# Optimization experiments

Hardware: AMD Instinct MI355X
Metric: run time of the kernel (lower is better)

Reference implementation:

```python
import jax, jax.numpy as jnp
import numpy as np


def setup_inputs() -> dict:
    key = jax.random.key(0)
    k1, k2 = jax.random.split(key)
    # [batch, seq, in_features] activations
    x = jax.random.normal(k1, (4, 4096, 2048), dtype=jnp.float32)
    # fp32 master weight [out_features, in_features]; quantized inside reference
    weight = jax.random.normal(k2, (2048, 2048), dtype=jnp.float32) * 0.02
    return {"x": x, "weight": weight}


def reference(x, weight):
    num_bits = 8
    Qn = -(2 ** (num_bits - 1))       # -128
    Qp = 2 ** (num_bits - 1) - 1      # 127

    # Per-row absmax int8 activation quantization (activation_quant)
    si = Qp / jnp.clip(jnp.max(jnp.abs(x), axis=-1, keepdims=True), 1e-5)  # [B,S,1]
    qx = jnp.clip(jnp.round(x * si), Qn, Qp)  # int8 values held in fp32 (exact)

    # Ternary weight quantization (weight_quant): sw scalar = 1/mean|W|
    sw = 1.0 / jnp.clip(jnp.mean(jnp.abs(weight)), 1e-5)
    qw = jnp.clip(jnp.round(weight * sw), -1.0, 1.0)  # {-1,0,1}

    acc = jnp.einsum("bsk,nk->bsn", qx, qw)  # [B,S,out]

    # post_quant_process: dequantize by si and sw, cast to half
    out = ((acc / si) / sw).astype(jnp.float16)
    return out
```

## Files before the change

kernel.cpp:

```cpp
#include <hip/hip_runtime.h>

#define K_DIM 2048
#define N_DIM 2048
#define M_DIM 16384

typedef int v4i __attribute__((ext_vector_type(4)));
typedef int v16i __attribute__((ext_vector_type(16)));


__device__ __forceinline__ void lds16(const void* g, void* l) {
    __builtin_amdgcn_global_load_lds(
        (const __attribute__((address_space(1))) unsigned int*)g,
        (__attribute__((address_space(3))) unsigned int*)l,
        16, 0, 0);
}

__global__ __launch_bounds__(256) void k_wsum(const float* __restrict__ w,
                                              double* __restrict__ part) {
    int tid = blockIdx.x * 256 + threadIdx.x;
    const float4* w4 = (const float4*)w;
    double s = 0.0;
    for (int i = tid; i < (N_DIM * K_DIM / 4); i += 65536) {
        float4 v = w4[i];
        s += (double)fabsf(v.x);
        s += (double)fabsf(v.y);
        s += (double)fabsf(v.z);
        s += (double)fabsf(v.w);
    }
#pragma unroll
    for (int off = 32; off; off >>= 1) s += __shfl_xor(s, off, 64);
    __shared__ double sp[4];
    int lane = threadIdx.x & 63, wv = threadIdx.x >> 6;
    if (lane == 0) sp[wv] = s;
    __syncthreads();
    if (threadIdx.x == 0) part[blockIdx.x] = sp[0] + sp[1] + sp[2] + sp[3];
}

__global__ __launch_bounds__(256) void k_quant_w(const float* __restrict__ w,
                                                 signed char* __restrict__ qw_t,
                                                 const double* __restrict__ part,
                                                 float* __restrict__ invsw_out) {
    double s = part[threadIdx.x];
#pragma unroll
    for (int off = 32; off; off >>= 1) s += __shfl_xor(s, off, 64);
    __shared__ double sp[4];
    __shared__ float s_invsw;
    int lane = threadIdx.x & 63, wv = threadIdx.x >> 6;
    if (lane == 0) sp[wv] = s;
    __syncthreads();
    if (threadIdx.x == 0) {
        double total = sp[0] + sp[1] + sp[2] + sp[3];
        float mean = (float)(total * (1.0 / (double)(N_DIM * K_DIM)));
        s_invsw = fmaxf(mean, 1e-5f);
        if (blockIdx.x == 0) *invsw_out = s_invsw;
    }
    __syncthreads();
    float sw = 1.0f / s_invsw;

    int row = blockIdx.x * 4 + wv;
    const float4* wr_ = (const float4*)(w + (size_t)row * K_DIM);
    int bn = row >> 7, ri = row & 127;
    signed char* base = qw_t + (size_t)bn * 262144 + (((lane >> 2) & 3) << 11) + (ri << 4) + ((lane & 3) << 2);
    int ksBase = lane >> 4;
#pragma unroll
    for (int c = 0; c < 8; c++) {
        float4 v = wr_[c * 64 + lane];
        int q0 = (int)fminf(fmaxf(rintf(v.x * sw), -1.f), 1.f);
        int q1 = (int)fminf(fmaxf(rintf(v.y * sw), -1.f), 1.f);
        int q2 = (int)fminf(fmaxf(rintf(v.z * sw), -1.f), 1.f);
        int q3 = (int)fminf(fmaxf(rintf(v.w * sw), -1.f), 1.f);
        int q = (q0 & 255) | ((q1 & 255) << 8) | ((q2 & 255) << 16) | ((q3 & 255) << 24);
        *(int*)(base + (size_t)(4 * c + ksBase) * 8192) = q;
    }
}

__global__ __launch_bounds__(256) void k_quant_x(const float* __restrict__ x,
                                                 signed char* __restrict__ qx_t,
                                                 float* __restrict__ si_out) {
    int row = blockIdx.x * 4 + (threadIdx.x >> 6);
    int lane = threadIdx.x & 63;
    const float4* xr = (const float4*)(x + (size_t)row * K_DIM);
    float4 v[8];
    float mx = 0.f;
#pragma unroll
    for (int c = 0; c < 8; c++) {
        v[c] = xr[c * 64 + lane];
        mx = fmaxf(mx, fmaxf(fmaxf(fabsf(v[c].x), fabsf(v[c].y)),
                             fmaxf(fabsf(v[c].z), fabsf(v[c].w))));
    }
#pragma unroll
    for (int off = 32; off; off >>= 1) mx = fmaxf(mx, __shfl_xor(mx, off, 64));
    float si = 127.0f / fmaxf(mx, 1e-5f);
    if (lane == 0) si_out[row] = si;

    int bm = row >> 8, ri = row & 255;
    signed char* base = qx_t + (size_t)bm * 524288 + (((lane >> 2) & 3) << 12) + (ri << 4) + ((lane & 3) << 2);
    int ksBase = lane >> 4;
#pragma unroll
    for (int c = 0; c < 8; c++) {
        int q0 = (int)fminf(fmaxf(rintf(v[c].x * si), -128.f), 127.f);
        int q1 = (int)fminf(fmaxf(rintf(v[c].y * si), -128.f), 127.f);
        int q2 = (int)fminf(fmaxf(rintf(v[c].z * si), -128.f), 127.f);
        int q3 = (int)fminf(fmaxf(rintf(v[c].w * si), -128.f), 127.f);
        int q = (q0 & 255) | ((q1 & 255) << 8) | ((q2 & 255) << 16) | ((q3 & 255) << 24);
        *(int*)(base + (size_t)(4 * c + ksBase) * 16384) = q;
    }
}

__global__ __launch_bounds__(256, 2) void k_gemm(const signed char* __restrict__ qx_t,
                                                 const signed char* __restrict__ qw_t,
                                                 const float* __restrict__ si,
                                                 const float* __restrict__ invsw_p,
                                                 float* __restrict__ out) {
    __shared__ __align__(16) signed char As[3][16384];
    __shared__ __align__(16) signed char Bs[2][8192];
    const int t = threadIdx.x;
    const int lane = t & 63, wv = t >> 6;
    const int wr = wv >> 1, wc = wv & 1;
    const int l31 = lane & 31, lh = lane >> 5;

    const int wg = blockIdx.x;
    const int swz = (wg & 7) * 128 + (wg >> 3);
    const int bn = swz & 15, bm = swz >> 4;

    const signed char* aT = qx_t + (size_t)bm * 524288;
    const signed char* bT = qw_t + (size_t)bn * 262144;
    const int t16 = t << 4;

#define STAGE_A(buf, ksv)                                    \
    {                                                        \
        const signed char* aS = aT + ((size_t)(ksv) << 14);  \
        signed char* Ad = As[buf];                           \
        lds16(aS + t16,         Ad + t16);                   \
        lds16(aS + 4096 + t16,  Ad + 4096 + t16);            \
        lds16(aS + 8192 + t16,  Ad + 8192 + t16);            \
        lds16(aS + 12288 + t16, Ad + 12288 + t16);           \
    }
#define STAGE_B(buf, ksv)                                    \
    {                                                        \
        const signed char* bS = bT + ((size_t)(ksv) << 13);  \
        signed char* Bd = Bs[buf];                           \
        lds16(bS + t16,         Bd + t16);                   \
        lds16(bS + 4096 + t16,  Bd + 4096 + t16);            \
    }

    v16i acc[4][2] = {};

#define COMPUTE(AC, BC)                                                                              \
    {                                                                                                \
        const signed char* Ac = As[AC];                                                              \
        const signed char* Bc = Bs[BC];                                                              \
        _Pragma("unroll")                                                                            \
        for (int ks2 = 0; ks2 < 2; ks2++) {                                                          \
            v4i af[4], bf[2];                                                                        \
            _Pragma("unroll")                                                                        \
            for (int mt = 0; mt < 4; mt++)                                                           \
                af[mt] = *(const v4i*)(Ac + (((ks2 * 2 + lh) * 256 + wr * 128 + mt * 32 + l31) << 4)); \
            _Pragma("unroll")                                                                        \
            for (int nt = 0; nt < 2; nt++)                                                           \
                bf[nt] = *(const v4i*)(Bc + (((ks2 * 2 + lh) * 128 + wc * 64 + nt * 32 + l31) << 4)); \
            _Pragma("unroll")                                                                        \
            for (int mt = 0; mt < 4; mt++)                                                           \
                _Pragma("unroll")                                                                    \
                for (int nt = 0; nt < 2; nt++)                                                       \
                    acc[mt][nt] = __builtin_amdgcn_mfma_i32_32x32x32_i8(af[mt], bf[nt], acc[mt][nt], 0, 0, 0); \
        }                                                                                            \
    }

#define ITER10(ksv, AC, BC, AS, BS)                          \
    {                                                        \
        STAGE_B(BS, (ksv) + 1);                              \
        STAGE_A(AS, (ksv) + 2);                              \
        asm volatile("s_waitcnt vmcnt(10)" ::: "memory");    \
        __builtin_amdgcn_s_barrier();                        \
        COMPUTE(AC, BC);                                     \
        __builtin_amdgcn_s_barrier();                        \
    }

    STAGE_B(0, 0);
    STAGE_A(0, 0);
    STAGE_A(1, 1);

    for (int ks = 0; ks < 30; ks += 6) {
        ITER10(ks + 0, 0, 0, 2, 1);
        ITER10(ks + 1, 1, 1, 0, 0);
        ITER10(ks + 2, 2, 0, 1, 1);
        ITER10(ks + 3, 0, 1, 2, 0);
        ITER10(ks + 4, 1, 0, 0, 1);
        ITER10(ks + 5, 2, 1, 1, 0);
    }

    STAGE_B(1, 31);
    asm volatile("s_waitcnt vmcnt(6)" ::: "memory");
    __builtin_amdgcn_s_barrier();
    COMPUTE(0, 0);
    __builtin_amdgcn_s_barrier();
    asm volatile("s_waitcnt vmcnt(0)" ::: "memory");
    __builtin_amdgcn_s_barrier();
    COMPUTE(1, 1);

#undef ITER10
#undef COMPUTE
#undef STAGE_A
#undef STAGE_B

    float invsw = *invsw_p;
#pragma unroll
    for (int mt = 0; mt < 4; mt++) {
        int rowb = bm * 256 + wr * 128 + mt * 32 + (lh << 2);
        float sc[16];
#pragma unroll
        for (int r = 0; r < 16; r++)
            sc[r] = invsw / si[rowb + (r & 3) + ((r >> 2) << 3)];
#pragma unroll
        for (int nt = 0; nt < 2; nt++) {
            int col = bn * 128 + wc * 64 + nt * 32 + l31;
#pragma unroll
            for (int r = 0; r < 16; r++) {
                int row = rowb + (r & 3) + ((r >> 2) << 3);
                float vv = (float)acc[mt][nt][r] * sc[r];
                out[(size_t)row * N_DIM + col] = (float)(_Float16)vv;
            }
        }
    }
}

extern "C" void kernel_launch(void* const* d_in, const int* in_sizes, int n_in,
                              void* d_out, int out_size, void* d_ws, size_t ws_size,
                              hipStream_t stream) {
    const float* x = (const float*)d_in[0];
    const float* w = (const float*)d_in[1];
    float* out = (float*)d_out;
    char* ws = (char*)d_ws;

    double* part = (double*)ws;
    float* invsw = (float*)(ws + 2048);
    float* si = (float*)(ws + 4096);
    signed char* qw_t = (signed char*)(ws + 4096 + 65536);
    signed char* qx_t = qw_t + (size_t)N_DIM * K_DIM;

    k_wsum<<<256, 256, 0, stream>>>(w, part);
    k_quant_x<<<4096, 256, 0, stream>>>(x, qx_t, si);
    k_quant_w<<<512, 256, 0, stream>>>(w, qw_t, part, invsw);
    k_gemm<<<1024, 256, 0, stream>>>(qx_t, qw_t, si, invsw, out);
}
```

Before: 323.2 us.

## Interleave LDS reads with MFMA in GEMM, coalesce quant stores, widen wsum grid

The GEMM main loop now uses a single barrier per k-step. It splits each step into two halves so the next tile's global-to-LDS loads are issued between the LDS fragment reads and the MFMAs, and it raises wave priority around the MFMA groups. Both quantization kernels first stage packed int8 words in shared memory, then write them out as contiguous runs in the tiled layout instead of scattered 4-byte stores. The weight-sum kernel runs with 4x more blocks, and the reducer sums four partials per thread. Removing the trailing barrier relies on the vmcnt wait plus the buffer rotation to avoid read/write races on LDS buffers.

```diff
diff --git a/kernel.cpp b/kernel.cpp
--- a/kernel.cpp
+++ b/kernel.cpp
@@ -20,7 +20,7 @@
     int tid = blockIdx.x * 256 + threadIdx.x;
     const float4* w4 = (const float4*)w;
     double s = 0.0;
-    for (int i = tid; i < (N_DIM * K_DIM / 4); i += 65536) {
+    for (int i = tid; i < (N_DIM * K_DIM / 4); i += 262144) {
         float4 v = w4[i];
         s += (double)fabsf(v.x);
         s += (double)fabsf(v.y);
@@ -40,11 +40,13 @@
                                                  signed char* __restrict__ qw_t,
                                                  const double* __restrict__ part,
                                                  float* __restrict__ invsw_out) {
-    double s = part[threadIdx.x];
+    double s = part[threadIdx.x] + part[threadIdx.x + 256] +
+               part[threadIdx.x + 512] + part[threadIdx.x + 768];
 #pragma unroll
     for (int off = 32; off; off >>= 1) s += __shfl_xor(s, off, 64);
     __shared__ double sp[4];
     __shared__ float s_invsw;
+    __shared__ int lbuf[2048];
     int lane = threadIdx.x & 63, wv = threadIdx.x >> 6;
     if (lane == 0) sp[wv] = s;
     __syncthreads();
@@ -59,9 +61,7 @@
 
     int row = blockIdx.x * 4 + wv;
     const float4* wr_ = (const float4*)(w + (size_t)row * K_DIM);
-    int bn = row >> 7, ri = row & 127;
-    signed char* base = qw_t + (size_t)bn * 262144 + (((lane >> 2) & 3) << 11) + (ri << 4) + ((lane & 3) << 2);
-    int ksBase = lane >> 4;
+    int k16 = (lane >> 2) & 3, b = lane & 3, ksBase = lane >> 4;
 #pragma unroll
     for (int c = 0; c < 8; c++) {
         float4 v = wr_[c * 64 + lane];
@@ -70,15 +70,28 @@
         int q2 = (int)fminf(fmaxf(rintf(v.z * sw), -1.f), 1.f);
         int q3 = (int)fminf(fmaxf(rintf(v.w * sw), -1.f), 1.f);
         int q = (q0 & 255) | ((q1 & 255) << 8) | ((q2 & 255) << 16) | ((q3 & 255) << 24);
-        *(int*)(base + (size_t)(4 * c + ksBase) * 8192) = q;
+        int ks = 4 * c + ksBase;
+        lbuf[(ks * 4 + k16) * 16 + wv * 4 + b] = q;
+    }
+    __syncthreads();
+    int bn = (blockIdx.x * 4) >> 7, ri0 = (blockIdx.x * 4) & 127;
+    int* qdst = (int*)(qw_t + (size_t)bn * 262144 + (size_t)ri0 * 16);
+#pragma unroll
+    for (int r = 0; r < 8; r++) {
+        int chunk = r * 16 + (threadIdx.x >> 4);
+        int i16 = threadIdx.x & 15;
+        int ks = chunk >> 2, kk = chunk & 3;
+        int row4 = i16 >> 2, bb = i16 & 3;
+        qdst[ks * 2048 + kk * 512 + row4 * 4 + bb] = lbuf[chunk * 16 + i16];
     }
 }
 
 __global__ __launch_bounds__(256) void k_quant_x(const float* __restrict__ x,
                                                  signed char* __restrict__ qx_t,
                                                  float* __restrict__ si_out) {
-    int row = blockIdx.x * 4 + (threadIdx.x >> 6);
-    int lane = threadIdx.x & 63;
+    __shared__ int lbuf[2048];
+    int wv = threadIdx.x >> 6, lane = threadIdx.x & 63;
+    int row = blockIdx.x * 4 + wv;
     const float4* xr = (const float4*)(x + (size_t)row * K_DIM);
     float4 v[8];
     float mx = 0.f;
@@ -93,9 +106,7 @@
     float si = 127.0f / fmaxf(mx, 1e-5f);
     if (lane == 0) si_out[row] = si;
 
-    int bm = row >> 8, ri = row & 255;
-    signed char* base = qx_t + (size_t)bm * 524288 + (((lane >> 2) & 3) << 12) + (ri << 4) + ((lane & 3) << 2);
-    int ksBase = lane >> 4;
+    int k16 = (lane >> 2) & 3, b = lane & 3, ksBase = lane >> 4;
 #pragma unroll
     for (int c = 0; c < 8; c++) {
         int q0 = (int)fminf(fmaxf(rintf(v[c].x * si), -128.f), 127.f);
@@ -103,7 +114,19 @@
         int q2 = (int)fminf(fmaxf(rintf(v[c].z * si), -128.f), 127.f);
         int q3 = (int)fminf(fmaxf(rintf(v[c].w * si), -128.f), 127.f);
         int q = (q0 & 255) | ((q1 & 255) << 8) | ((q2 & 255) << 16) | ((q3 & 255) << 24);
-        *(int*)(base + (size_t)(4 * c + ksBase) * 16384) = q;
+        int ks = 4 * c + ksBase;
+        lbuf[(ks * 4 + k16) * 16 + wv * 4 + b] = q;
+    }
+    __syncthreads();
+    int bm = (blockIdx.x * 4) >> 8, ri0 = (blockIdx.x * 4) & 255;
+    int* qdst = (int*)(qx_t + (size_t)bm * 524288 + (size_t)ri0 * 16);
+#pragma unroll
+    for (int r = 0; r < 8; r++) {
+        int chunk = r * 16 + (threadIdx.x >> 4);
+        int i16 = threadIdx.x & 15;
+        int ks = chunk >> 2, kk = chunk & 3;
+        int row4 = i16 >> 2, bb = i16 & 3;
+        qdst[ks * 4096 + kk * 1024 + row4 * 4 + bb] = lbuf[chunk * 16 + i16];
     }
 }
 
@@ -146,35 +169,31 @@
 
     v16i acc[4][2] = {};
 
-#define COMPUTE(AC, BC)                                                                              \
-    {                                                                                                \
-        const signed char* Ac = As[AC];                                                              \
-        const signed char* Bc = Bs[BC];                                                              \
-        _Pragma("unroll")                                                                            \
-        for (int ks2 = 0; ks2 < 2; ks2++) {                                                          \
-            v4i af[4], bf[2];                                                                        \
-            _Pragma("unroll")                                                                        \
-            for (int mt = 0; mt < 4; mt++)                                                           \
-                af[mt] = *(const v4i*)(Ac + (((ks2 * 2 + lh) * 256 + wr * 128 + mt * 32 + l31) << 4)); \
-            _Pragma("unroll")                                                                        \
-            for (int nt = 0; nt < 2; nt++)                                                           \
-                bf[nt] = *(const v4i*)(Bc + (((ks2 * 2 + lh) * 128 + wc * 64 + nt * 32 + l31) << 4)); \
-            _Pragma("unroll")                                                                        \
-            for (int mt = 0; mt < 4; mt++)                                                           \
-                _Pragma("unroll")                                                                    \
-                for (int nt = 0; nt < 2; nt++)                                                       \
-                    acc[mt][nt] = __builtin_amdgcn_mfma_i32_32x32x32_i8(af[mt], bf[nt], acc[mt][nt], 0, 0, 0); \
-        }                                                                                            \
-    }
-
-#define ITER10(ksv, AC, BC, AS, BS)                          \
+#define READ_HALF(AC, BC, h, af, bf)                                                                 \
+    _Pragma("unroll") for (int mt = 0; mt < 4; mt++)                                                 \
+        af[mt] = *(const v4i*)(As[AC] + ((((h) * 2 + lh) * 256 + wr * 128 + mt * 32 + l31) << 4));   \
+    _Pragma("unroll") for (int nt = 0; nt < 2; nt++)                                                 \
+        bf[nt] = *(const v4i*)(Bs[BC] + ((((h) * 2 + lh) * 128 + wc * 64 + nt * 32 + l31) << 4));
+
+#define MFMA8(af, bf)                                                                                \
+    __builtin_amdgcn_s_setprio(1);                                                                   \
+    _Pragma("unroll") for (int mt = 0; mt < 4; mt++)                                                 \
+        _Pragma("unroll") for (int nt = 0; nt < 2; nt++)                                             \
+            acc[mt][nt] = __builtin_amdgcn_mfma_i32_32x32x32_i8(af[mt], bf[nt], acc[mt][nt], 0, 0, 0); \
+    __builtin_amdgcn_s_setprio(0);
+
+#define ITER(ksv, AC, BC, AS, BS)                            \
     {                                                        \
+        asm volatile("s_waitcnt vmcnt(4)" ::: "memory");     \
+        __builtin_amdgcn_s_barrier();                        \
+        __builtin_amdgcn_sched_barrier(0);                   \
+        v4i af[4], bf[2];                                    \
+        READ_HALF(AC, BC, 0, af, bf);                        \
         STAGE_B(BS, (ksv) + 1);                              \
+        MFMA8(af, bf);                                       \
+        READ_HALF(AC, BC, 1, af, bf);                        \
         STAGE_A(AS, (ksv) + 2);                              \
-        asm volatile("s_waitcnt vmcnt(10)" ::: "memory");    \
-        __builtin_amdgcn_s_barrier();                        \
-        COMPUTE(AC, BC);                                     \
-        __builtin_amdgcn_s_barrier();                        \
+        MFMA8(af, bf);                                       \
     }
 
     STAGE_B(0, 0);
@@ -182,25 +201,39 @@
     STAGE_A(1, 1);
 
     for (int ks = 0; ks < 30; ks += 6) {
-        ITER10(ks + 0, 0, 0, 2, 1);
-        ITER10(ks + 1, 1, 1, 0, 0);
-        ITER10(ks + 2, 2, 0, 1, 1);
-        ITER10(ks + 3, 0, 1, 2, 0);
-        ITER10(ks + 4, 1, 0, 0, 1);
-        ITER10(ks + 5, 2, 1, 1, 0);
-    }
-
-    STAGE_B(1, 31);
-    asm volatile("s_waitcnt vmcnt(6)" ::: "memory");
-    __builtin_amdgcn_s_barrier();
-    COMPUTE(0, 0);
-    __builtin_amdgcn_s_barrier();
-    asm volatile("s_waitcnt vmcnt(0)" ::: "memory");
-    __builtin_amdgcn_s_barrier();
-    COMPUTE(1, 1);
-
-#undef ITER10
-#undef COMPUTE
+        ITER(ks + 0, 0, 0, 2, 1);
+        ITER(ks + 1, 1, 1, 0, 0);
+        ITER(ks + 2, 2, 0, 1, 1);
+        ITER(ks + 3, 0, 1, 2, 0);
+        ITER(ks + 4, 1, 0, 0, 1);
+        ITER(ks + 5, 2, 1, 1, 0);
+    }
+
+    {
+        asm volatile("s_waitcnt vmcnt(4)" ::: "memory");
+        __builtin_amdgcn_s_barrier();
+        __builtin_amdgcn_sched_barrier(0);
+        v4i af[4], bf[2];
+        READ_HALF(0, 0, 0, af, bf);
+        STAGE_B(1, 31);
+        MFMA8(af, bf);
+        READ_HALF(0, 0, 1, af, bf);
+        MFMA8(af, bf);
+    }
+    {
+        asm volatile("s_waitcnt vmcnt(0)" ::: "memory");
+        __builtin_amdgcn_s_barrier();
+        __builtin_amdgcn_sched_barrier(0);
+        v4i af[4], bf[2];
+        READ_HALF(1, 1, 0, af, bf);
+        MFMA8(af, bf);
+        READ_HALF(1, 1, 1, af, bf);
+        MFMA8(af, bf);
+    }
+
+#undef ITER
+#undef MFMA8
+#undef READ_HALF
 #undef STAGE_A
 #undef STAGE_B
 
@@ -234,12 +267,12 @@
     char* ws = (char*)d_ws;
 
     double* part = (double*)ws;
-    float* invsw = (float*)(ws + 2048);
-    float* si = (float*)(ws + 4096);
-    signed char* qw_t = (signed char*)(ws + 4096 + 65536);
+    float* invsw = (float*)(ws + 8192);
+    float* si = (float*)(ws + 12288);
+    signed char* qw_t = (signed char*)(ws + 12288 + 65536);
     signed char* qx_t = qw_t + (size_t)N_DIM * K_DIM;
 
-    k_wsum<<<256, 256, 0, stream>>>(w, part);
+    k_wsum<<<1024, 256, 0, stream>>>(w, part);
     k_quant_x<<<4096, 256, 0, stream>>>(x, qx_t, si);
     k_quant_w<<<512, 256, 0, stream>>>(w, qw_t, part, invsw);
     k_gemm<<<1024, 256, 0, stream>>>(qx_t, qw_t, si, invsw, out);
```

Measured after the change: 312.7 us. 1.03x faster.
